# Optimization experiments

Measured on AMD Instinct MI355X. Metric: run time of the kernel, lower is better.

The kernel has to match this reference:

```python
import jax, jax.numpy as jnp
import numpy as np

B, S, H = 2, 1024, 2048
NH, NKV, HD = 32, 8, 64          # head_dim = H // NH
G = NH // NKV                    # GQA group size = 4
THETA = 500000.0
EPS = 1e-5
SCALE = HD ** -0.5


def _rope_neox(x, positions):
    # x: [B, S, n_heads, HD]; neox style: rotate concatenated halves
    inv_freq = 1.0 / (THETA ** (jnp.arange(0, HD, 2, dtype=jnp.float32) / HD))  # [HD/2]
    ang = positions[..., None].astype(jnp.float32) * inv_freq                    # [B, S, HD/2]
    cos = jnp.cos(ang)[:, :, None, :]
    sin = jnp.sin(ang)[:, :, None, :]
    x1, x2 = jnp.split(x, 2, axis=-1)
    return jnp.concatenate([x1 * cos - x2 * sin, x2 * cos + x1 * sin], axis=-1)


def setup_inputs() -> dict:
    key = jax.random.key(0)
    k1, k2, k3 = jax.random.split(key, 3)
    hidden_states = jax.random.normal(k1, (B, S, H), jnp.float32)
    w_qkv = jax.random.normal(k2, ((NH + 2 * NKV) * HD, H), jnp.float32) * 0.02
    w_o = jax.random.normal(k3, (H, NH * HD), jnp.float32) * 0.02
    norm_w = jnp.ones((H,), jnp.float32)
    positions = jnp.broadcast_to(jnp.arange(S, dtype=jnp.int32), (B, S))
    return {"hidden_states": hidden_states, "positions": positions,
            "w_qkv": w_qkv, "w_o": w_o, "norm_w": norm_w}


def reference(hidden_states, positions, w_qkv, w_o, norm_w):
    # QKV projection (bias=False) and split
    qkv = hidden_states @ w_qkv.T                                 # [B,S,3072]
    q, k, v = jnp.split(qkv, [NH * HD, NH * HD + NKV * HD], axis=-1)
    q = q.reshape(B, S, NH, HD)
    k = k.reshape(B, S, NKV, HD)
    v = v.reshape(B, S, NKV, HD)

    # RoPE on q and k (full rotary_dim = head_dim)
    q = _rope_neox(q, positions)
    k = _rope_neox(k, positions)

    # Causal GQA attention (dense-prefill equivalent of RadixAttention)
    qg = q.reshape(B, S, NKV, G, HD)
    scores = jnp.einsum('bqhgd,bkhd->bhgqk', qg, k) * SCALE       # [B,NKV,G,S,S]
    causal = jnp.tril(jnp.ones((S, S), dtype=bool))
    scores = jnp.where(causal, scores, jnp.float32(-1e30))
    probs = jax.nn.softmax(scores, axis=-1)
    attn = jnp.einsum('bhgqk,bkhd->bqhgd', probs, v).reshape(B, S, NH * HD)

    # BitNet sub-norm (RMSNorm) then output projection
    var = jnp.mean(attn * attn, axis=-1, keepdims=True)
    normed = attn * jax.lax.rsqrt(var + EPS) * norm_w
    return normed @ w_o.T                                         # [B,S,H]
```

## Files before the change

kernel.cpp:

```cpp
#include <hip/hip_runtime.h>
#include <hip/hip_bf16.h>
#include <cstdint>
#include <cstddef>

typedef __bf16 bf16;
typedef __bf16 bf16x2 __attribute__((ext_vector_type(2)));
typedef __bf16 bf16x4 __attribute__((ext_vector_type(4)));
typedef __bf16 bf16x8 __attribute__((ext_vector_type(8)));
typedef float  f32x4  __attribute__((ext_vector_type(4)));

__device__ __forceinline__ void async_copy16(const void* g, void* l) {
  __builtin_amdgcn_global_load_lds((const __attribute__((address_space(1))) void*)g,
                                   (__attribute__((address_space(3))) void*)l,
                                   16, 0, 0);
}

__device__ __forceinline__ int swz(int row) { return ((row >> 1) & 3) << 3; }

__device__ __forceinline__ bool block_flag_is_f32(const unsigned int* w, int tid,
                                                  int* sflag) {
  if (tid < 64) {
    int weird = 0;
#pragma unroll
    for (int c = 0; c < 2; ++c) {
      const unsigned int lo = w[c * 64 + tid] & 0xffffu;
      const unsigned int ex = (lo >> 7) & 0xffu;
      if (ex >= 134u) ++weird;
    }
    const unsigned long long m1 = __ballot(weird >= 1);
    const unsigned long long m2 = __ballot(weird == 2);
    if (tid == 0) *sflag = (__popcll(m1) + __popcll(m2) >= 8) ? 1 : 0;
  }
  __syncthreads();
  return *sflag != 0;
}

__global__ __launch_bounds__(256) void convert_all(
    const void* __restrict__ s0, const void* __restrict__ s1,
    const void* __restrict__ s2, const void* __restrict__ s3,
    bf16* __restrict__ d0, bf16* __restrict__ d1, bf16* __restrict__ d2,
    float* __restrict__ ssum) {
  __shared__ int sflag;
  const int tid = threadIdx.x;
  const bool f32 = block_flag_is_f32((const unsigned int*)s0, tid, &sflag);
  if (blockIdx.x == 0) {
    ((float4*)ssum)[tid * 2]     = make_float4(0.f, 0.f, 0.f, 0.f);
    ((float4*)ssum)[tid * 2 + 1] = make_float4(0.f, 0.f, 0.f, 0.f);
  }
  const int i = blockIdx.x * 256 + tid;
  if (i >= 3670016) return;
  const void* src; bf16* dst; int off; bool fold = false;
  if      (i < 1048576) { src = s0; dst = d0; off = i; }
  else if (i < 2621440) { src = s1; dst = d1; off = i - 1048576; }
  else                  { src = s2; dst = d2; off = i - 2621440; fold = true; }
  float v[4];
  if (f32) {
    const float4 t = ((const float4*)src)[off];
    v[0] = t.x; v[1] = t.y; v[2] = t.z; v[3] = t.w;
  } else {
    const bf16x4 t = ((const bf16x4*)src)[off];
#pragma unroll
    for (int j = 0; j < 4; ++j) v[j] = (float)t[j];
  }
  if (fold) {
    const int k0 = (off * 4) & 2047;
#pragma unroll
    for (int j = 0; j < 4; ++j) {
      const float w = f32 ? ((const float*)s3)[k0 + j] : (float)((const bf16*)s3)[k0 + j];
      v[j] *= w;
    }
  }
  bf16x4 o;
#pragma unroll
  for (int j = 0; j < 4; ++j) o[j] = (bf16)v[j];
  *(bf16x4*)(dst + (size_t)off * 4) = o;
}

__global__ __launch_bounds__(256) void gemm_qkv_rope(
    const bf16* __restrict__ A, const bf16* __restrict__ B,
    const int* __restrict__ pos,
    bf16* __restrict__ Q, bf16* __restrict__ K, bf16* __restrict__ V)
{
  __shared__ __align__(16) bf16 As[4 * 64 * 32];
  __shared__ __align__(16) bf16 Bs[4 * 128 * 32];
  const int tid = threadIdx.x, wave = tid >> 6, lane = tid & 63;
  const int l15 = lane & 15, l4 = lane >> 4;
  const int m0 = blockIdx.y * 64, n0 = blockIdx.x * 128;
  const int wm = (wave >> 1) * 32, wn = (wave & 1) * 64;
  const int KD = 2048;
  const int swz_ro = (l4 * 8) ^ swz(l15);

  f32x4 acc[2][4] = {};

  for (int kt = 0; kt < KD; kt += 128) {
#pragma unroll
    for (int c = 0; c < 4; ++c) {
      const int e = c * 2048 + tid * 8;
      const int kc = e >> 11, row = (e >> 5) & 63;
      const int o = (e & 31) ^ swz(row);
      async_copy16(A + (size_t)(m0 + row) * KD + kt + kc * 32 + o, As + e);
    }
#pragma unroll
    for (int c = 0; c < 8; ++c) {
      const int e = c * 2048 + tid * 8;
      const int kc = e >> 12, row = (e >> 5) & 127;
      const int o = (e & 31) ^ swz(row);
      async_copy16(B + (size_t)(n0 + row) * KD + kt + kc * 32 + o, Bs + e);
    }
    __syncthreads();
#pragma unroll
    for (int s = 0; s < 4; ++s) {
      bf16x8 af[2], bfr[4];
#pragma unroll
      for (int i = 0; i < 2; ++i)
        af[i] = *(const bf16x8*)(As + s * 2048 + (wm + i * 16 + l15) * 32 + swz_ro);
#pragma unroll
      for (int j = 0; j < 4; ++j)
        bfr[j] = *(const bf16x8*)(Bs + s * 4096 + (wn + j * 16 + l15) * 32 + swz_ro);
#pragma unroll
      for (int i = 0; i < 2; ++i)
#pragma unroll
        for (int j = 0; j < 4; ++j)
          acc[i][j] = __builtin_amdgcn_mfma_f32_16x16x32_bf16(af[i], bfr[j], acc[i][j], 0, 0, 0);
    }
    __syncthreads();
  }

  if (n0 < 2560) {
    const bool isQ = (n0 < 2048);
#pragma unroll
    for (int i = 0; i < 2; ++i)
#pragma unroll
      for (int j = 0; j < 4; ++j) {
        const int col = n0 + wn + j * 16 + l15;
        const int hd = isQ ? col : (col - 2048);
        const int hh = hd >> 6, d = hd & 63;
        const int fi = d & 31;
        const float ifr = __expf((float)fi * -0.41007385554f);
#pragma unroll
        for (int r = 0; r < 4; ++r) {
          const int m = m0 + wm + i * 16 + l4 * 4 + r;
          const int b = m >> 10, s = m & 1023;
          const float ang = (float)pos[m] * ifr;
          float sn, cs;
          __sincosf(ang, &sn, &cs);
          const float x  = acc[i][j][r];
          const float xp = acc[i][j ^ 2][r];
          const float v = (d < 32) ? (x * cs - xp * sn) : (x * cs + xp * sn);
          if (isQ) Q[(((size_t)(b * 32 + hh)) * 1024 + s) * 64 + d] = (bf16)(v * 0.125f);
          else     K[(((size_t)(b * 8 + hh)) * 1024 + s) * 64 + d] = (bf16)v;
        }
      }
  } else {
#pragma unroll
    for (int i = 0; i < 2; ++i)
#pragma unroll
      for (int j = 0; j < 4; ++j) {
        const int cv = n0 + wn + j * 16 + l15 - 2560;
        const int hh = cv >> 6, d = cv & 63;
#pragma unroll
        for (int r = 0; r < 4; ++r) {
          const int m = m0 + wm + i * 16 + l4 * 4 + r;
          const int b = m >> 10, s = m & 1023;
          const int sp = (s & ~31) + ((s & 15) * 2 + ((s >> 4) & 1));
          V[(((size_t)(b * 8 + hh)) * 64 + d) * 1024 + sp] = (bf16)acc[i][j][r];
        }
      }
  }
}

__global__ __launch_bounds__(256) void attn_kernel(
    const bf16* __restrict__ Q, const bf16* __restrict__ K,
    const bf16* __restrict__ Vt, bf16* __restrict__ O, float* __restrict__ ssum)
{
  __shared__ __align__(16) bf16 Ks[2 * 128 * 32];
  __shared__ __align__(16) bf16 Vs[4 * 64 * 32];
  __shared__ __align__(16) bf16 Ps[4 * 128 * 40];

  const int tid = threadIdx.x, wave = tid >> 6, lane = tid & 63;
  const int l15 = lane & 15, l4 = lane >> 4;
  const int swz_ro = (l4 * 8) ^ swz(l15);
  const int ip = blockIdx.x, bh = blockIdx.y;
  const int b = bh >> 5, h = bh & 31, kvh = h >> 2;
  const int qlo = ip * 64, qhi = (15 - ip) * 64;
  const bf16* Qb = Q + ((size_t)(b * 32 + h)) * 65536;
  const bf16* Kb = K + ((size_t)(b * 8 + kvh)) * 65536;
  const bf16* Vb = Vt + ((size_t)(b * 8 + kvh)) * 65536;

#pragma unroll
  for (int c = 0; c < 4; ++c) {
    const int e = c * 2048 + tid * 8;
    const int dchunk = e >> 12;
    const int row = (e & 4095) >> 5;
    const int qb = (row < 64) ? qlo : qhi;
    const int o = (e & 31) ^ swz(row);
    async_copy16(Qb + (size_t)(qb + (row & 63)) * 64 + dchunk * 32 + o, Ps + e);
  }
  __syncthreads();
  bf16x8 aq[2][2];
#pragma unroll
  for (int i = 0; i < 2; ++i)
#pragma unroll
    for (int s = 0; s < 2; ++s)
      aq[i][s] = *(const bf16x8*)(Ps + s * 4096 + (i * 64 + wave * 16 + l15) * 32 + swz_ro);
  __syncthreads();

  float m_s[2][4], l_s[2][4];
  f32x4 o_acc[2][4] = {};
#pragma unroll
  for (int i = 0; i < 2; ++i)
#pragma unroll
    for (int r = 0; r < 4; ++r) { m_s[i][r] = -3.0e4f; l_s[i][r] = 0.f; }

  const int nkt = (1151 - 64 * ip) >> 7;
  for (int kt = 0; kt < nkt; ++kt) {
    const int k0 = kt * 128;
    const bool lo_act = (k0 < (ip + 1) * 64);
#pragma unroll
    for (int c = 0; c < 4; ++c) {
      const int e = c * 2048 + tid * 8;
      const int krow = (e & 4095) >> 5;
      const int ko = (e & 31) ^ swz(krow);
      async_copy16(Kb + (size_t)(k0 + krow) * 64 + (e >> 12) * 32 + ko, Ks + e);
      const int drow = (e & 2047) >> 5;
      const int vo = (e & 31) ^ swz(drow);
      async_copy16(Vb + (size_t)drow * 1024 + k0 + (e >> 11) * 32 + vo, Vs + e);
    }
    __syncthreads();

    f32x4 sc[2][8] = {};
#pragma unroll
    for (int j = 0; j < 8; ++j) {
      const bf16x8 bk0 = *(const bf16x8*)(Ks + (j * 16 + l15) * 32 + swz_ro);
      const bf16x8 bk1 = *(const bf16x8*)(Ks + 4096 + (j * 16 + l15) * 32 + swz_ro);
      sc[1][j] = __builtin_amdgcn_mfma_f32_16x16x32_bf16(aq[1][0], bk0, sc[1][j], 0, 0, 0);
      sc[1][j] = __builtin_amdgcn_mfma_f32_16x16x32_bf16(aq[1][1], bk1, sc[1][j], 0, 0, 0);
      if (lo_act) {
        sc[0][j] = __builtin_amdgcn_mfma_f32_16x16x32_bf16(aq[0][0], bk0, sc[0][j], 0, 0, 0);
        sc[0][j] = __builtin_amdgcn_mfma_f32_16x16x32_bf16(aq[0][1], bk1, sc[0][j], 0, 0, 0);
      }
    }

#pragma unroll
    for (int hh = 0; hh < 2; ++hh) {
      if (hh == 0 && !lo_act) continue;
      const int qb = hh ? qhi : qlo;
#pragma unroll
      for (int r = 0; r < 4; ++r) {
        const int rl = wave * 16 + l4 * 4 + r;
        const int rg = qb + rl;
        float mx = -3.0e4f;
#pragma unroll
        for (int j = 0; j < 8; ++j) {
          float v = sc[hh][j][r];
          if (k0 + j * 16 + l15 > rg) v = -3.0e4f;
          sc[hh][j][r] = v;
          mx = fmaxf(mx, v);
        }
#pragma unroll
        for (int off = 1; off < 16; off <<= 1) mx = fmaxf(mx, __shfl_xor(mx, off));
        const float mnew = fmaxf(m_s[hh][r], mx);
        const float alpha = __expf(m_s[hh][r] - mnew);
        m_s[hh][r] = mnew;
        float rs = 0.f;
#pragma unroll
        for (int t = 0; t < 4; ++t) {
          const float pv0 = __expf(sc[hh][2 * t][r]     - mnew);
          const float pv1 = __expf(sc[hh][2 * t + 1][r] - mnew);
          rs += pv0 + pv1;
          bf16x2 pk; pk[0] = (bf16)pv0; pk[1] = (bf16)pv1;
          *(bf16x2*)(Ps + t * 5120 + (hh * 64 + rl) * 40 + l15 * 2) = pk;
        }
#pragma unroll
        for (int off = 1; off < 16; off <<= 1) rs += __shfl_xor(rs, off);
        l_s[hh][r] = l_s[hh][r] * alpha + rs;
#pragma unroll
        for (int jd = 0; jd < 4; ++jd) o_acc[hh][jd][r] *= alpha;
      }
    }

#pragma unroll
    for (int ks = 0; ks < 4; ++ks) {
      bf16x8 bv[4];
#pragma unroll
      for (int jd = 0; jd < 4; ++jd)
        bv[jd] = *(const bf16x8*)(Vs + ks * 2048 + (jd * 16 + l15) * 32 + swz_ro);
#pragma unroll
      for (int hh = 0; hh < 2; ++hh) {
        if (hh == 0 && !lo_act) continue;
        const bf16x8 ap = *(const bf16x8*)(Ps + ks * 5120 + (hh * 64 + wave * 16 + l15) * 40 + l4 * 8);
#pragma unroll
        for (int jd = 0; jd < 4; ++jd)
          o_acc[hh][jd] = __builtin_amdgcn_mfma_f32_16x16x32_bf16(ap, bv[jd], o_acc[hh][jd], 0, 0, 0);
      }
    }
    __syncthreads();
  }

#pragma unroll
  for (int hh = 0; hh < 2; ++hh) {
    const int qb = hh ? qhi : qlo;
#pragma unroll
    for (int r = 0; r < 4; ++r) {
      const float inv = 1.0f / l_s[hh][r];
      const int srow = qb + wave * 16 + l4 * 4 + r;
      bf16* op = O + ((size_t)(b * 1024 + srow)) * 2048 + h * 64;
      float ss = 0.f;
#pragma unroll
      for (int jd = 0; jd < 4; ++jd) {
        const float v = o_acc[hh][jd][r] * inv;
        op[jd * 16 + l15] = (bf16)v;
        ss += v * v;
      }
#pragma unroll
      for (int off = 1; off < 16; off <<= 1) ss += __shfl_xor(ss, off);
      if (l15 == 0) atomicAdd(&ssum[b * 1024 + srow], ss);
    }
  }
}

__global__ __launch_bounds__(256) void gemm_out(
    const bf16* __restrict__ A, const bf16* __restrict__ B,
    const float* __restrict__ ssum, const unsigned int* __restrict__ hs_raw,
    void* __restrict__ out)
{
  __shared__ __align__(16) bf16 As[4 * 64 * 32];
  __shared__ __align__(16) bf16 Bs[4 * 128 * 32];
  __shared__ int sflag;
  const int tid = threadIdx.x, wave = tid >> 6, lane = tid & 63;
  const bool f32out = block_flag_is_f32(hs_raw, tid, &sflag);
  const int l15 = lane & 15, l4 = lane >> 4;
  const int m0 = blockIdx.y * 64, n0 = blockIdx.x * 128;
  const int wm = (wave >> 1) * 32, wn = (wave & 1) * 64;
  const int KD = 2048;
  const int swz_ro = (l4 * 8) ^ swz(l15);

  f32x4 acc[2][4] = {};

  for (int kt = 0; kt < KD; kt += 128) {
#pragma unroll
    for (int c = 0; c < 4; ++c) {
      const int e = c * 2048 + tid * 8;
      const int kc = e >> 11, row = (e >> 5) & 63;
      const int o = (e & 31) ^ swz(row);
      async_copy16(A + (size_t)(m0 + row) * KD + kt + kc * 32 + o, As + e);
    }
#pragma unroll
    for (int c = 0; c < 8; ++c) {
      const int e = c * 2048 + tid * 8;
      const int kc = e >> 12, row = (e >> 5) & 127;
      const int o = (e & 31) ^ swz(row);
      async_copy16(B + (size_t)(n0 + row) * KD + kt + kc * 32 + o, Bs + e);
    }
    __syncthreads();
#pragma unroll
    for (int s = 0; s < 4; ++s) {
      bf16x8 af[2], bfr[4];
#pragma unroll
      for (int i = 0; i < 2; ++i)
        af[i] = *(const bf16x8*)(As + s * 2048 + (wm + i * 16 + l15) * 32 + swz_ro);
#pragma unroll
      for (int j = 0; j < 4; ++j)
        bfr[j] = *(const bf16x8*)(Bs + s * 4096 + (wn + j * 16 + l15) * 32 + swz_ro);
#pragma unroll
      for (int i = 0; i < 2; ++i)
#pragma unroll
        for (int j = 0; j < 4; ++j)
          acc[i][j] = __builtin_amdgcn_mfma_f32_16x16x32_bf16(af[i], bfr[j], acc[i][j], 0, 0, 0);
    }
    __syncthreads();
  }

#pragma unroll
  for (int i = 0; i < 2; ++i)
#pragma unroll
    for (int r = 0; r < 4; ++r) {
      const int row = m0 + wm + i * 16 + l4 * 4 + r;
      const float ri = rsqrtf(ssum[row] * (1.0f / 2048.0f) + 1e-5f);
#pragma unroll
      for (int j = 0; j < 4; ++j) {
        const int col = n0 + wn + j * 16 + l15;
        const size_t idx = (size_t)row * 2048 + col;
        const float v = ri * acc[i][j][r];
        if (f32out) ((float*)out)[idx] = v;
        else        ((bf16*)out)[idx]  = (bf16)v;
      }
    }
}

extern "C" void kernel_launch(void* const* d_in, const int* in_sizes, int n_in,
                              void* d_out, int out_size, void* d_ws, size_t ws_size,
                              hipStream_t stream) {
  const void* hs     = d_in[0];
  const int*  pos    = (const int*)d_in[1];
  const void* w_qkv  = d_in[2];
  const void* w_o    = d_in[3];
  const void* norm_w = d_in[4];

  char* ws = (char*)d_ws;
  bf16*  hs_b   = (bf16*) (ws);
  bf16*  wqkv_b = (bf16*) (ws + 8388608);
  bf16*  w_o_b  = (bf16*) (ws + 20971520);
  float* ssum   = (float*)(ws + 29360128);
  bf16*  Qr     = (bf16*) (ws + 29368320);
  bf16*  Kr     = (bf16*) (ws + 37756928);
  bf16*  Vtr    = (bf16*) (ws + 39854080);
  bf16*  attn_o = (bf16*) (ws + 41951232);

  convert_all<<<14336, 256, 0, stream>>>(hs, w_qkv, w_o, norm_w,
                                         hs_b, wqkv_b, w_o_b, ssum);
  gemm_qkv_rope<<<dim3(24, 32), 256, 0, stream>>>(hs_b, wqkv_b, pos, Qr, Kr, Vtr);
  attn_kernel<<<dim3(8, 64), 256, 0, stream>>>(Qr, Kr, Vtr, attn_o, ssum);
  gemm_out<<<dim3(16, 32), 256, 0, stream>>>(attn_o, w_o_b, ssum,
                                             (const unsigned int*)hs, d_out);
}
```

Measured before the change: 205.3 us.

## Remap block IDs for XCD locality, grid-stride convert, exp2 softmax, skip masks

Launches become 1D grids, and block IDs are remapped so that consecutive blocks on each of the 8 XCDs share A/B tiles or KV heads, with the aim of better L2 reuse. The conversion kernel processes four elements per thread with a quarter as many blocks. The softmax folds log2(e) into the Q scale so it can use exp2f instead of __expf, and it skips causal masking on tiles that lie fully below the diagonal. These are several unrelated changes bundled together. The remap only helps if the hardware dispatches blocks round-robin across XCDs as assumed.

```diff
diff --git a/kernel.cpp b/kernel.cpp
--- a/kernel.cpp
+++ b/kernel.cpp
@@ -47,33 +47,35 @@
     ((float4*)ssum)[tid * 2]     = make_float4(0.f, 0.f, 0.f, 0.f);
     ((float4*)ssum)[tid * 2 + 1] = make_float4(0.f, 0.f, 0.f, 0.f);
   }
-  const int i = blockIdx.x * 256 + tid;
-  if (i >= 3670016) return;
-  const void* src; bf16* dst; int off; bool fold = false;
-  if      (i < 1048576) { src = s0; dst = d0; off = i; }
-  else if (i < 2621440) { src = s1; dst = d1; off = i - 1048576; }
-  else                  { src = s2; dst = d2; off = i - 2621440; fold = true; }
-  float v[4];
-  if (f32) {
-    const float4 t = ((const float4*)src)[off];
-    v[0] = t.x; v[1] = t.y; v[2] = t.z; v[3] = t.w;
-  } else {
-    const bf16x4 t = ((const bf16x4*)src)[off];
-#pragma unroll
-    for (int j = 0; j < 4; ++j) v[j] = (float)t[j];
-  }
-  if (fold) {
-    const int k0 = (off * 4) & 2047;
-#pragma unroll
-    for (int j = 0; j < 4; ++j) {
-      const float w = f32 ? ((const float*)s3)[k0 + j] : (float)((const bf16*)s3)[k0 + j];
-      v[j] *= w;
-    }
-  }
-  bf16x4 o;
-#pragma unroll
-  for (int j = 0; j < 4; ++j) o[j] = (bf16)v[j];
-  *(bf16x4*)(dst + (size_t)off * 4) = o;
+#pragma unroll
+  for (int k = 0; k < 4; ++k) {
+    const int i = blockIdx.x * 256 + tid + k * 917504;
+    const void* src; bf16* dst; int off; bool fold = false;
+    if      (i < 1048576) { src = s0; dst = d0; off = i; }
+    else if (i < 2621440) { src = s1; dst = d1; off = i - 1048576; }
+    else                  { src = s2; dst = d2; off = i - 2621440; fold = true; }
+    float v[4];
+    if (f32) {
+      const float4 t = ((const float4*)src)[off];
+      v[0] = t.x; v[1] = t.y; v[2] = t.z; v[3] = t.w;
+    } else {
+      const bf16x4 t = ((const bf16x4*)src)[off];
+#pragma unroll
+      for (int j = 0; j < 4; ++j) v[j] = (float)t[j];
+    }
+    if (fold) {
+      const int k0 = (off * 4) & 2047;
+#pragma unroll
+      for (int j = 0; j < 4; ++j) {
+        const float w = f32 ? ((const float*)s3)[k0 + j] : (float)((const bf16*)s3)[k0 + j];
+        v[j] *= w;
+      }
+    }
+    bf16x4 o;
+#pragma unroll
+    for (int j = 0; j < 4; ++j) o[j] = (bf16)v[j];
+    *(bf16x4*)(dst + (size_t)off * 4) = o;
+  }
 }
 
 __global__ __launch_bounds__(256) void gemm_qkv_rope(
@@ -85,7 +87,9 @@
   __shared__ __align__(16) bf16 Bs[4 * 128 * 32];
   const int tid = threadIdx.x, wave = tid >> 6, lane = tid & 63;
   const int l15 = lane & 15, l4 = lane >> 4;
-  const int m0 = blockIdx.y * 64, n0 = blockIdx.x * 128;
+  const int bid = blockIdx.x;
+  const int sid = (bid & 7) * 96 + (bid >> 3);
+  const int m0 = (sid & 31) * 64, n0 = (sid >> 5) * 128;
   const int wm = (wave >> 1) * 32, wn = (wave & 1) * 64;
   const int KD = 2048;
   const int swz_ro = (l4 * 8) ^ swz(l15);
@@ -147,7 +151,7 @@
           const float x  = acc[i][j][r];
           const float xp = acc[i][j ^ 2][r];
           const float v = (d < 32) ? (x * cs - xp * sn) : (x * cs + xp * sn);
-          if (isQ) Q[(((size_t)(b * 32 + hh)) * 1024 + s) * 64 + d] = (bf16)(v * 0.125f);
+          if (isQ) Q[(((size_t)(b * 32 + hh)) * 1024 + s) * 64 + d] = (bf16)(v * 0.1803368801f);
           else     K[(((size_t)(b * 8 + hh)) * 1024 + s) * 64 + d] = (bf16)v;
         }
       }
@@ -180,8 +184,11 @@
   const int tid = threadIdx.x, wave = tid >> 6, lane = tid & 63;
   const int l15 = lane & 15, l4 = lane >> 4;
   const int swz_ro = (l4 * 8) ^ swz(l15);
-  const int ip = blockIdx.x, bh = blockIdx.y;
-  const int b = bh >> 5, h = bh & 31, kvh = h >> 2;
+  const int bid = blockIdx.x;
+  const int sid = (bid & 7) * 64 + (bid >> 3);
+  const int chunk = sid >> 5, inner = sid & 31;
+  const int b = chunk >> 3, kvh = chunk & 7;
+  const int h = kvh * 4 + (inner >> 3), ip = inner & 7;
   const int qlo = ip * 64, qhi = (15 - ip) * 64;
   const bf16* Qb = Q + ((size_t)(b * 32 + h)) * 65536;
   const bf16* Kb = K + ((size_t)(b * 8 + kvh)) * 65536;
@@ -245,28 +252,34 @@
     for (int hh = 0; hh < 2; ++hh) {
       if (hh == 0 && !lo_act) continue;
       const int qb = hh ? qhi : qlo;
+      const bool need_mask = (k0 + 127 > qb + wave * 16);
 #pragma unroll
       for (int r = 0; r < 4; ++r) {
         const int rl = wave * 16 + l4 * 4 + r;
         const int rg = qb + rl;
         float mx = -3.0e4f;
-#pragma unroll
-        for (int j = 0; j < 8; ++j) {
-          float v = sc[hh][j][r];
-          if (k0 + j * 16 + l15 > rg) v = -3.0e4f;
-          sc[hh][j][r] = v;
-          mx = fmaxf(mx, v);
+        if (need_mask) {
+#pragma unroll
+          for (int j = 0; j < 8; ++j) {
+            float v = sc[hh][j][r];
+            if (k0 + j * 16 + l15 > rg) v = -3.0e4f;
+            sc[hh][j][r] = v;
+            mx = fmaxf(mx, v);
+          }
+        } else {
+#pragma unroll
+          for (int j = 0; j < 8; ++j) mx = fmaxf(mx, sc[hh][j][r]);
         }
 #pragma unroll
         for (int off = 1; off < 16; off <<= 1) mx = fmaxf(mx, __shfl_xor(mx, off));
         const float mnew = fmaxf(m_s[hh][r], mx);
-        const float alpha = __expf(m_s[hh][r] - mnew);
+        const float alpha = exp2f(m_s[hh][r] - mnew);
         m_s[hh][r] = mnew;
         float rs = 0.f;
 #pragma unroll
         for (int t = 0; t < 4; ++t) {
-          const float pv0 = __expf(sc[hh][2 * t][r]     - mnew);
-          const float pv1 = __expf(sc[hh][2 * t + 1][r] - mnew);
+          const float pv0 = exp2f(sc[hh][2 * t][r]     - mnew);
+          const float pv1 = exp2f(sc[hh][2 * t + 1][r] - mnew);
           rs += pv0 + pv1;
           bf16x2 pk; pk[0] = (bf16)pv0; pk[1] = (bf16)pv1;
           *(bf16x2*)(Ps + t * 5120 + (hh * 64 + rl) * 40 + l15 * 2) = pk;
@@ -330,7 +343,9 @@
   const int tid = threadIdx.x, wave = tid >> 6, lane = tid & 63;
   const bool f32out = block_flag_is_f32(hs_raw, tid, &sflag);
   const int l15 = lane & 15, l4 = lane >> 4;
-  const int m0 = blockIdx.y * 64, n0 = blockIdx.x * 128;
+  const int bid = blockIdx.x;
+  const int sid = (bid & 7) * 64 + (bid >> 3);
+  const int m0 = (sid & 31) * 64, n0 = (sid >> 5) * 128;
   const int wm = (wave >> 1) * 32, wn = (wave & 1) * 64;
   const int KD = 2048;
   const int swz_ro = (l4 * 8) ^ swz(l15);
@@ -407,10 +422,10 @@
   bf16*  Vtr    = (bf16*) (ws + 39854080);
   bf16*  attn_o = (bf16*) (ws + 41951232);
 
-  convert_all<<<14336, 256, 0, stream>>>(hs, w_qkv, w_o, norm_w,
-                                         hs_b, wqkv_b, w_o_b, ssum);
-  gemm_qkv_rope<<<dim3(24, 32), 256, 0, stream>>>(hs_b, wqkv_b, pos, Qr, Kr, Vtr);
-  attn_kernel<<<dim3(8, 64), 256, 0, stream>>>(Qr, Kr, Vtr, attn_o, ssum);
-  gemm_out<<<dim3(16, 32), 256, 0, stream>>>(attn_o, w_o_b, ssum,
-                                             (const unsigned int*)hs, d_out);
-}
+  convert_all<<<3584, 256, 0, stream>>>(hs, w_qkv, w_o, norm_w,
+                                        hs_b, wqkv_b, w_o_b, ssum);
+  gemm_qkv_rope<<<768, 256, 0, stream>>>(hs_b, wqkv_b, pos, Qr, Kr, Vtr);
+  attn_kernel<<<512, 256, 0, stream>>>(Qr, Kr, Vtr, attn_o, ssum);
+  gemm_out<<<512, 256, 0, stream>>>(attn_o, w_o_b, ssum,
+                                    (const unsigned int*)hs, d_out);
+}
```

Measured after the change: 213.3 us. 3.9% more time.
